# Optimization experiments

Measured on AMD Instinct MI355X. Metric: run time of the kernel, lower is better.

Reference implementation:

```python
import jax, jax.numpy as jnp
import numpy as np
import math

B, S, H = 8, 2048, 256

def setup_inputs() -> dict:
    key = jax.random.key(0)
    ks = jax.random.split(key, 7)
    stdv = 1.0 / math.sqrt(H)
    return {
        "k": jax.random.normal(ks[0], (B, S, H), dtype=jnp.float32),
        "q": jax.random.normal(ks[1], (B, S, H), dtype=jnp.float32),
        "v": jax.random.normal(ks[2], (B, S, H), dtype=jnp.float32),
        "mask": jax.random.bernoulli(ks[3], 0.5, (B, S, S)),  # bool, masked-out positions
        "W_query": jax.random.uniform(ks[4], (H, H), jnp.float32, -stdv, stdv),
        "W_key": jax.random.uniform(ks[5], (H, H), jnp.float32, -stdv, stdv),
        "W_val": jax.random.uniform(ks[6], (H, H), jnp.float32, -stdv, stdv),
    }

def reference(k, q, v, mask, W_query, W_key, W_val):
    Q = jnp.einsum("bsh,hd->bsd", q, W_query)
    K = jnp.einsum("bsh,hd->bsd", k, W_key)
    V = jnp.einsum("bsh,hd->bsd", v, W_val)
    norm = 1.0 / math.sqrt(Q.shape[-1])
    compat = norm * jnp.einsum("bqd,bkd->bqk", Q, K)  # [B,Sq,Sk]
    compat = jnp.where(mask, -jnp.inf, compat)
    score = jax.nn.softmax(compat, axis=-1)
    score = jnp.nan_to_num(score, nan=0.0)  # fully-masked rows -> all zeros
    return jnp.einsum("bqk,bkd->bqd", score, V)
```

## Files before the change

### kernel.cpp

```cpp
#include <hip/hip_runtime.h>


#define B_ 8
#define S_ 2048
#define H_ 256

typedef __attribute__((ext_vector_type(8))) short s16x8;
typedef __attribute__((ext_vector_type(4))) float f32x4;
typedef __attribute__((ext_vector_type(4))) unsigned short u16x4;
typedef __attribute__((ext_vector_type(8))) unsigned short u16x8;

#if __has_builtin(__builtin_amdgcn_exp2f)
#define EXP2F(x) __builtin_amdgcn_exp2f(x)
#else
#define EXP2F(x) exp2f(x)
#endif
#define L2E 1.4426950408889634f

__device__ __forceinline__ unsigned short f2bf(float f) {
  unsigned int u = __builtin_bit_cast(unsigned int, f);
  u += 0x7fffu + ((u >> 16) & 1u);
  return (unsigned short)(u >> 16);
}
__device__ __forceinline__ float bf2f(unsigned short h) {
  unsigned int u = ((unsigned int)h) << 16;
  return __builtin_bit_cast(float, u);
}
__device__ __forceinline__ f32x4 mfma_bf16(s16x8 a, s16x8 b, f32x4 c) {
  return __builtin_amdgcn_mfma_f32_16x16x32_bf16(a, b, c, 0, 0, 0);
}
__device__ __forceinline__ float sel4(const float v[4], int r) {
  float t0 = (r & 1) ? v[1] : v[0];
  float t1 = (r & 1) ? v[3] : v[2];
  return (r & 2) ? t1 : t0;
}
__device__ __forceinline__ void async16(const unsigned short* g, unsigned short* l) {
  __builtin_amdgcn_global_load_lds(
      (const __attribute__((address_space(1))) unsigned int*)g,
      (__attribute__((address_space(3))) unsigned int*)l, 16, 0, 0);
}

__global__ __launch_bounds__(256) void wt_kernel(
    const float* __restrict__ Wq, const float* __restrict__ Wk,
    const float* __restrict__ Wv, unsigned short* __restrict__ Wt) {
  __shared__ unsigned short tile[64 * 72];
  int z = blockIdx.x >> 4, x = blockIdx.x & 15;
  const float* W = (z == 0) ? Wq : (z == 1) ? Wk : Wv;
  int n0 = (x & 3) * 64, h0 = (x >> 2) * 64;
  int t = threadIdx.x;
#pragma unroll
  for (int j = 0; j < 4; ++j) {
    int c = j * 256 + t;
    int i = c >> 4, ch = c & 15;
    float4 f = *(const float4*)&W[(h0 + i) * 256 + n0 + ch * 4];
    u16x4 p;
    p[0] = f2bf(f.x); p[1] = f2bf(f.y); p[2] = f2bf(f.z); p[3] = f2bf(f.w);
    *(u16x4*)&tile[i * 72 + ch * 4] = p;
  }
  __syncthreads();
#pragma unroll
  for (int j = 0; j < 2; ++j) {
    int c = j * 256 + t;
    int nr = c >> 3, ch = c & 7;
    u16x8 o;
#pragma unroll
    for (int k = 0; k < 8; ++k) o[k] = tile[(ch * 8 + k) * 72 + nr];
    *(u16x8*)&Wt[z * 65536 + (n0 + nr) * 256 + h0 + ch * 8] = o;
  }
}

__global__ __launch_bounds__(256) void fused_kernel(
    const int* __restrict__ mask, unsigned short* __restrict__ Mb,
    const float* __restrict__ Xq, const float* __restrict__ Xk,
    const float* __restrict__ Xv, const unsigned short* __restrict__ Wt,
    unsigned short* __restrict__ Qb, unsigned short* __restrict__ Kb,
    unsigned short* __restrict__ Vt) {
  __shared__ unsigned short plds[16384];

  if (blockIdx.x >= 768) {
    unsigned int g = (blockIdx.x - 768) * 256 + threadIdx.x;
    const int4* src = (const int4*)mask + (size_t)g * 4;
    unsigned int v = 0;
#pragma unroll
    for (int j = 0; j < 4; ++j) {
      int4 x = src[j];
      v |= (x.x != 0 ? 1u : 0u) << (j * 4 + 0);
      v |= (x.y != 0 ? 1u : 0u) << (j * 4 + 1);
      v |= (x.z != 0 ? 1u : 0u) << (j * 4 + 2);
      v |= (x.w != 0 ? 1u : 0u) << (j * 4 + 3);
    }
    Mb[g] = (unsigned short)v;
    return;
  }

  int z = blockIdx.x >> 8;
  int bx = blockIdx.x & 255;
  const float* X = (z == 0) ? Xq : (z == 1) ? Xk : Xv;
  const unsigned short* Wz = Wt + z * 65536;

  int t = threadIdx.x;
  int w = t >> 6, lane = t & 63, quad = lane >> 4, l15 = lane & 15;
  int m0 = bx * 64;
  const float* xrow = X + (size_t)(m0 + w * 16 + l15) * H_;

  f32x4 zero4 = {0.f, 0.f, 0.f, 0.f};
  f32x4 acc[16];
#pragma unroll
  for (int i = 0; i < 16; ++i) acc[i] = zero4;

#pragma unroll
  for (int j = 0; j < 4; ++j) {
    int c = j * 256 + t;
    int n = c >> 2, p = c & 3;
    async16(Wz + n * 256 + ((p ^ ((n >> 1) & 3)) << 3),
            plds + j * 2048 + w * 512);
  }
  float4 a0 = *(const float4*)(xrow + quad * 8);
  float4 a1 = *(const float4*)(xrow + quad * 8 + 4);

  for (int c8 = 0; c8 < 8; ++c8) {
    int cur = c8 & 1;
    unsigned short* Wc = plds + cur * 8192;
    __syncthreads();

    if (c8 < 7) {
      unsigned short* Wn = plds + (cur ^ 1) * 8192;
#pragma unroll
      for (int j = 0; j < 4; ++j) {
        int c = j * 256 + t;
        int n = c >> 2, p = c & 3;
        async16(Wz + n * 256 + (c8 + 1) * 32 + ((p ^ ((n >> 1) & 3)) << 3),
                Wn + j * 2048 + w * 512);
      }
    }
    float4 na0, na1;
    if (c8 < 7) {
      na0 = *(const float4*)(xrow + (c8 + 1) * 32 + quad * 8);
      na1 = *(const float4*)(xrow + (c8 + 1) * 32 + quad * 8 + 4);
    }
    s16x8 af;
    af[0] = (short)f2bf(a0.x); af[1] = (short)f2bf(a0.y);
    af[2] = (short)f2bf(a0.z); af[3] = (short)f2bf(a0.w);
    af[4] = (short)f2bf(a1.x); af[5] = (short)f2bf(a1.y);
    af[6] = (short)f2bf(a1.z); af[7] = (short)f2bf(a1.w);

#pragma unroll
    for (int nf = 0; nf < 16; ++nf) {
      int n = nf * 16 + l15;
      s16x8 bf = *(const s16x8*)&Wc[n * 32 + ((quad ^ ((n >> 1) & 3)) << 3)];
      acc[nf] = mfma_bf16(af, bf, acc[nf]);
    }
    a0 = na0; a1 = na1;
  }
  __syncthreads();

  float scale = (z == 0) ? 0.0625f : 1.0f;
  int b = m0 >> 11, s0 = m0 & 2047;
#pragma unroll
  for (int h = 0; h < 2; ++h) {
    if (h) __syncthreads();
    if (z < 2) {
#pragma unroll
      for (int nf2 = 0; nf2 < 8; ++nf2) {
        int n = nf2 * 16 + l15;
#pragma unroll
        for (int r = 0; r < 4; ++r)
          plds[(w * 16 + quad * 4 + r) * 136 + n] = f2bf(acc[h * 8 + nf2][r] * scale);
      }
      __syncthreads();
      unsigned short* Y = (z == 0) ? Qb : Kb;
#pragma unroll
      for (int j = 0; j < 4; ++j) {
        int c = j * 256 + t;
        int mr = c >> 4, ch = c & 15;
        u16x8 o = *(const u16x8*)&plds[mr * 136 + ch * 8];
        *(u16x8*)&Y[(size_t)(m0 + mr) * H_ + h * 128 + ch * 8] = o;
      }
    } else {
#pragma unroll
      for (int nf2 = 0; nf2 < 8; ++nf2) {
        int dl = nf2 * 16 + l15;
#pragma unroll
        for (int r = 0; r < 4; ++r)
          plds[dl * 72 + (w * 16 + quad * 4 + r)] = f2bf(acc[h * 8 + nf2][r]);
      }
      __syncthreads();
#pragma unroll
      for (int j = 0; j < 4; ++j) {
        int c = j * 256 + t;
        int dr = c >> 3, ch = c & 7;
        u16x8 o = *(const u16x8*)&plds[dr * 72 + ch * 8];
        *(u16x8*)&Vt[((size_t)b * H_ + h * 128 + dr) * S_ + s0 + ch * 8] = o;
      }
    }
  }
}

__global__ __launch_bounds__(256, 2) void attn_kernel(
    const unsigned short* __restrict__ Qb, const unsigned short* __restrict__ Kb,
    const unsigned short* __restrict__ Vt, const unsigned int* __restrict__ Mb,
    unsigned short* __restrict__ Op, float* __restrict__ Ml,
    float* __restrict__ out) {
  __shared__ unsigned short lds[35328];
  unsigned short* Ps = lds + 32768;

  int t = threadIdx.x;
  int w = t >> 6, lane = t & 63, quad = lane >> 4, l15 = lane & 15;
  int b = blockIdx.x;
  int q0 = blockIdx.y * 64;
  int split = blockIdx.z, nsplit = gridDim.z;
  int kbeg = (64 * split) / nsplit, kend = (64 * (split + 1)) / nsplit;

  s16x8 qa[8];
  {
    const unsigned short* qp =
        Qb + ((size_t)b * S_ + q0 + w * 16 + l15) * H_ + quad * 8;
#pragma unroll
    for (int c = 0; c < 8; ++c) qa[c] = *(const s16x8*)(qp + 32 * c);
  }

  const unsigned short* Kbb = Kb + (size_t)b * S_ * H_;
  const unsigned short* Vbb = Vt + (size_t)b * H_ * S_;

  int krow = lane >> 5, kch = lane & 31;
  int vrow = lane >> 2, vch = lane & 3;

  f32x4 zero4 = {0.f, 0.f, 0.f, 0.f};
  f32x4 acc[16];
#pragma unroll
  for (int i = 0; i < 16; ++i) acc[i] = zero4;
  float l_r[4] = {0.f, 0.f, 0.f, 0.f};

  const unsigned int* mrow[4];
#pragma unroll
  for (int r = 0; r < 4; ++r)
    mrow[r] = Mb + ((size_t)b * S_ + q0 + w * 16 + quad * 4 + r) * 64;

  {
    int k0 = kbeg * 32;
    unsigned short* Kd = lds;
    unsigned short* Vd = lds + 8192;
#pragma unroll
    for (int j = 0; j < 4; ++j) {
      int key = (w * 4 + j) * 2 + krow;
      async16(Kbb + ((size_t)(k0 + key) << 8) + ((kch ^ (key & 7)) << 3),
              Kd + (w * 4 + j) * 512);
      int d = w * 64 + j * 16 + vrow;
      async16(Vbb + ((size_t)d << 11) + k0 + ((vch ^ (d & 3)) << 3),
              Vd + (w * 64 + j * 16) * 32);
    }
  }
  unsigned int mw[4];
#pragma unroll
  for (int r = 0; r < 4; ++r) mw[r] = mrow[r][kbeg];

  for (int kt = kbeg; kt < kend; ++kt) {
    int cur = (kt - kbeg) & 1;
    unsigned short* Ksc = lds + cur * 16384;
    unsigned short* Vsc = Ksc + 8192;
    __syncthreads();

    if (kt + 1 < kend) {
      int k0 = (kt + 1) * 32;
      unsigned short* Kd = lds + (cur ^ 1) * 16384;
      unsigned short* Vd = Kd + 8192;
#pragma unroll
      for (int j = 0; j < 4; ++j) {
        int key = (w * 4 + j) * 2 + krow;
        async16(Kbb + ((size_t)(k0 + key) << 8) + ((kch ^ (key & 7)) << 3),
                Kd + (w * 4 + j) * 512);
        int d = w * 64 + j * 16 + vrow;
        async16(Vbb + ((size_t)d << 11) + k0 + ((vch ^ (d & 3)) << 3),
                Vd + (w * 64 + j * 16) * 32);
      }
    }
    unsigned int mwn[4];
    {
      int ktn = (kt + 1 < kend) ? kt + 1 : kt;
#pragma unroll
      for (int r = 0; r < 4; ++r) mwn[r] = mrow[r][ktn];
    }

    f32x4 sacc[2];
#pragma unroll
    for (int nf = 0; nf < 2; ++nf) sacc[nf] = zero4;
#pragma unroll
    for (int c = 0; c < 8; ++c) {
#pragma unroll
      for (int nf = 0; nf < 2; ++nf) {
        int n = nf * 16 + l15;
        s16x8 kb = *(const s16x8*)&Ksc[n * 256 + (((quad + 4 * c) ^ (n & 7)) << 3)];
        sacc[nf] = mfma_bf16(qa[c], kb, sacc[nf]);
      }
    }

    float pvv[2][4];
#pragma unroll
    for (int r = 0; r < 4; ++r) {
      unsigned int bits = mw[r] >> l15;
#pragma unroll
      for (int nf = 0; nf < 2; ++nf) {
        float p = ((bits >> (nf * 16)) & 1u)
                      ? 0.f
                      : EXP2F(sacc[nf][r] * L2E);
        pvv[nf][r] = p;
        l_r[r] += p;
      }
    }

#pragma unroll
    for (int nf = 0; nf < 2; ++nf)
#pragma unroll
      for (int r = 0; r < 4; ++r) {
        int key = nf * 16 + l15;
        int ql = quad * 4 + r;
        Ps[w * 640 + ql * 40 + key] = f2bf(pvv[nf][r]);
      }

    {
      s16x8 bp = *(const s16x8*)&Ps[w * 640 + l15 * 40 + quad * 8];
#pragma unroll
      for (int mf = 0; mf < 16; ++mf) {
        int d = mf * 16 + l15;
        s16x8 av = *(const s16x8*)&Vsc[d * 32 + ((quad ^ (d & 3)) << 3)];
        acc[mf] = mfma_bf16(av, bp, acc[mf]);
      }
    }

#pragma unroll
    for (int r = 0; r < 4; ++r) mw[r] = mwn[r];
  }

#pragma unroll
  for (int r = 0; r < 4; ++r) {
#pragma unroll
    for (int d = 1; d < 16; d <<= 1) l_r[r] += __shfl_xor(l_r[r], d, 64);
  }

  if (gridDim.z == 1) {
    float l4[4];
    int srcl = (l15 >> 2) << 4;
#pragma unroll
    for (int r = 0; r < 4; ++r) l4[r] = __shfl(l_r[r], srcl, 64);
    float lq = sel4(l4, l15 & 3);
    float linv = (lq > 0.f) ? (1.0f / lq) : 0.f;
    float* op = out + ((size_t)b * S_ + q0 + w * 16 + l15) * H_ + quad * 4;
#pragma unroll
    for (int mf = 0; mf < 16; ++mf) {
      float4 o;
      o.x = acc[mf][0] * linv; o.y = acc[mf][1] * linv;
      o.z = acc[mf][2] * linv; o.w = acc[mf][3] * linv;
      *(float4*)(op + mf * 16) = o;
    }
  } else {
    int qg = q0 + w * 16 + l15;
    unsigned short* op =
        Op + (((size_t)split * B_ + b) * S_ + qg) * H_ + quad * 4;
#pragma unroll
    for (int mf = 0; mf < 16; ++mf) {
      u16x4 pk;
      pk[0] = f2bf(acc[mf][0]); pk[1] = f2bf(acc[mf][1]);
      pk[2] = f2bf(acc[mf][2]); pk[3] = f2bf(acc[mf][3]);
      *(u16x4*)(op + mf * 16) = pk;
    }
    if (l15 == 0) {
#pragma unroll
      for (int r = 0; r < 4; ++r) {
        int qr = q0 + w * 16 + quad * 4 + r;
        Ml[((size_t)split * B_ + b) * S_ + qr] = l_r[r];
      }
    }
  }
}

__global__ __launch_bounds__(1024) void combine_kernel(
    const unsigned short* __restrict__ Op, const float* __restrict__ Ml,
    float* __restrict__ out, int nsplit) {
  int q = blockIdx.x * 4 + (threadIdx.x >> 8);
  int b = blockIdx.y, d = threadIdx.x & 255;
  float osum = 0.f, lsum = 0.f;
  for (int i = 0; i < nsplit; ++i) {
    size_t ro = ((size_t)i * B_ + b) * S_ + q;
    lsum += Ml[ro];
    osum += bf2f(Op[ro * H_ + d]);
  }
  float linv = (lsum > 0.f) ? (1.0f / lsum) : 0.f;
  out[((size_t)b * S_ + q) * H_ + d] = osum * linv;
}

extern "C" void kernel_launch(void* const* d_in, const int* in_sizes, int n_in,
                              void* d_out, int out_size, void* d_ws, size_t ws_size,
                              hipStream_t stream) {
  const float* k_in = (const float*)d_in[0];
  const float* q_in = (const float*)d_in[1];
  const float* v_in = (const float*)d_in[2];
  const int* mask = (const int*)d_in[3];
  const float* Wq = (const float*)d_in[4];
  const float* Wk = (const float*)d_in[5];
  const float* Wv = (const float*)d_in[6];
  float* out = (float*)d_out;

  unsigned short* Qb = (unsigned short*)d_ws;
  unsigned short* Kb = Qb + (size_t)4194304;
  unsigned short* Vt = Kb + (size_t)4194304;
  unsigned short* Wt = Vt + (size_t)4194304;
  unsigned short* Mb = Wt + (size_t)196608;
  unsigned short* Op = Mb + (size_t)2097152;
  float* Ml = (float*)(Op + (size_t)8388608);
  const size_t need = 46792704;
  int nsplit = (ws_size >= need) ? 2 : 1;

  hipLaunchKernelGGL(wt_kernel, dim3(48), dim3(256), 0, stream,
                     Wq, Wk, Wv, Wt);
  hipLaunchKernelGGL(fused_kernel, dim3(8960), dim3(256), 0, stream,
                     mask, Mb, q_in, k_in, v_in, Wt, Qb, Kb, Vt);
  hipLaunchKernelGGL(attn_kernel, dim3(8, 32, nsplit), dim3(256), 0, stream,
                     Qb, Kb, Vt, (const unsigned int*)Mb, Op, Ml, out);
  if (nsplit > 1)
    hipLaunchKernelGGL(combine_kernel, dim3(512, 8), dim3(1024), 0, stream,
                       Op, Ml, out, nsplit);
}
```

Before: 311.2 us.

## Read int mask directly in attention kernel instead of pre-packing bits

Removes the bit-packing pass over the int32 mask that ran inside the projection kernel, and has the attention kernel load the raw int mask entries per lane. The intent is to drop a full extra pass over the 128MB mask and the extra launch work. The cost is that the attention kernel now reads four bytes per mask entry instead of one bit, with stride-S row loads per lane, which may add memory traffic to the attention loop. The mask is still read only once overall.

```diff
diff --git a/kernel.cpp b/kernel.cpp
--- a/kernel.cpp
+++ b/kernel.cpp
@@ -69,30 +69,13 @@
   }
 }
 
-__global__ __launch_bounds__(256) void fused_kernel(
-    const int* __restrict__ mask, unsigned short* __restrict__ Mb,
+__global__ __launch_bounds__(256) void proj_kernel(
     const float* __restrict__ Xq, const float* __restrict__ Xk,
     const float* __restrict__ Xv, const unsigned short* __restrict__ Wt,
     unsigned short* __restrict__ Qb, unsigned short* __restrict__ Kb,
     unsigned short* __restrict__ Vt) {
   __shared__ unsigned short plds[16384];
 
-  if (blockIdx.x >= 768) {
-    unsigned int g = (blockIdx.x - 768) * 256 + threadIdx.x;
-    const int4* src = (const int4*)mask + (size_t)g * 4;
-    unsigned int v = 0;
-#pragma unroll
-    for (int j = 0; j < 4; ++j) {
-      int4 x = src[j];
-      v |= (x.x != 0 ? 1u : 0u) << (j * 4 + 0);
-      v |= (x.y != 0 ? 1u : 0u) << (j * 4 + 1);
-      v |= (x.z != 0 ? 1u : 0u) << (j * 4 + 2);
-      v |= (x.w != 0 ? 1u : 0u) << (j * 4 + 3);
-    }
-    Mb[g] = (unsigned short)v;
-    return;
-  }
-
   int z = blockIdx.x >> 8;
   int bx = blockIdx.x & 255;
   const float* X = (z == 0) ? Xq : (z == 1) ? Xk : Xv;
@@ -198,7 +181,7 @@
 
 __global__ __launch_bounds__(256, 2) void attn_kernel(
     const unsigned short* __restrict__ Qb, const unsigned short* __restrict__ Kb,
-    const unsigned short* __restrict__ Vt, const unsigned int* __restrict__ Mb,
+    const unsigned short* __restrict__ Vt, const int* __restrict__ mask,
     unsigned short* __restrict__ Op, float* __restrict__ Ml,
     float* __restrict__ out) {
   __shared__ unsigned short lds[35328];
@@ -231,10 +214,10 @@
   for (int i = 0; i < 16; ++i) acc[i] = zero4;
   float l_r[4] = {0.f, 0.f, 0.f, 0.f};
 
-  const unsigned int* mrow[4];
+  const int* mrowp[4];
 #pragma unroll
   for (int r = 0; r < 4; ++r)
-    mrow[r] = Mb + ((size_t)b * S_ + q0 + w * 16 + quad * 4 + r) * 64;
+    mrowp[r] = mask + ((size_t)b * S_ + q0 + w * 16 + quad * 4 + r) * S_;
 
   {
     int k0 = kbeg * 32;
@@ -250,9 +233,12 @@
               Vd + (w * 64 + j * 16) * 32);
     }
   }
-  unsigned int mw[4];
-#pragma unroll
-  for (int r = 0; r < 4; ++r) mw[r] = mrow[r][kbeg];
+  int mw[2][4];
+#pragma unroll
+  for (int nf = 0; nf < 2; ++nf)
+#pragma unroll
+    for (int r = 0; r < 4; ++r)
+      mw[nf][r] = mrowp[r][kbeg * 32 + nf * 16 + l15];
 
   for (int kt = kbeg; kt < kend; ++kt) {
     int cur = (kt - kbeg) & 1;
@@ -274,11 +260,14 @@
                 Vd + (w * 64 + j * 16) * 32);
       }
     }
-    unsigned int mwn[4];
+    int mwn[2][4];
     {
       int ktn = (kt + 1 < kend) ? kt + 1 : kt;
 #pragma unroll
-      for (int r = 0; r < 4; ++r) mwn[r] = mrow[r][ktn];
+      for (int nf = 0; nf < 2; ++nf)
+#pragma unroll
+        for (int r = 0; r < 4; ++r)
+          mwn[nf][r] = mrowp[r][ktn * 32 + nf * 16 + l15];
     }
 
     f32x4 sacc[2];
@@ -297,12 +286,9 @@
     float pvv[2][4];
 #pragma unroll
     for (int r = 0; r < 4; ++r) {
-      unsigned int bits = mw[r] >> l15;
 #pragma unroll
       for (int nf = 0; nf < 2; ++nf) {
-        float p = ((bits >> (nf * 16)) & 1u)
-                      ? 0.f
-                      : EXP2F(sacc[nf][r] * L2E);
+        float p = mw[nf][r] ? 0.f : EXP2F(sacc[nf][r] * L2E);
         pvv[nf][r] = p;
         l_r[r] += p;
       }
@@ -328,7 +314,9 @@
     }
 
 #pragma unroll
-    for (int r = 0; r < 4; ++r) mw[r] = mwn[r];
+    for (int nf = 0; nf < 2; ++nf)
+#pragma unroll
+      for (int r = 0; r < 4; ++r) mw[nf][r] = mwn[nf][r];
   }
 
 #pragma unroll
@@ -404,18 +392,17 @@
   unsigned short* Kb = Qb + (size_t)4194304;
   unsigned short* Vt = Kb + (size_t)4194304;
   unsigned short* Wt = Vt + (size_t)4194304;
-  unsigned short* Mb = Wt + (size_t)196608;
-  unsigned short* Op = Mb + (size_t)2097152;
+  unsigned short* Op = Wt + (size_t)196608;
   float* Ml = (float*)(Op + (size_t)8388608);
-  const size_t need = 46792704;
+  const size_t need = 42467328;
   int nsplit = (ws_size >= need) ? 2 : 1;
 
   hipLaunchKernelGGL(wt_kernel, dim3(48), dim3(256), 0, stream,
                      Wq, Wk, Wv, Wt);
-  hipLaunchKernelGGL(fused_kernel, dim3(8960), dim3(256), 0, stream,
-                     mask, Mb, q_in, k_in, v_in, Wt, Qb, Kb, Vt);
+  hipLaunchKernelGGL(proj_kernel, dim3(768), dim3(256), 0, stream,
+                     q_in, k_in, v_in, Wt, Qb, Kb, Vt);
   hipLaunchKernelGGL(attn_kernel, dim3(8, 32, nsplit), dim3(256), 0, stream,
-                     Qb, Kb, Vt, (const unsigned int*)Mb, Op, Ml, out);
+                     Qb, Kb, Vt, mask, Op, Ml, out);
   if (nsplit > 1)
     hipLaunchKernelGGL(combine_kernel, dim3(512, 8), dim3(1024), 0, stream,
                        Op, Ml, out, nsplit);
```

After: 293.0 us. 5.8% less time.
